# Kernel tuning notes

Hardware: AMD Instinct MI355X
Metric: run time of the kernel (lower is better)

Reference implementation:

```python
import jax, jax.numpy as jnp
import numpy as np

B, C, T = 128, 9, 2048
R = T // 4            # reduced_timesteps after two MaxPool1d(2)
N = B * R             # total graph nodes
E_SINGLE = 8192       # edges per sample graph (avg degree 16 over R nodes)
HID = 128
OUT = 12


def setup_inputs():
    key = jax.random.key(0)
    ks = jax.random.split(key, 14)
    x = jax.random.normal(ks[0], (B, C, T), jnp.float32)
    # per-sample graph, replicated with offset i*R per batch element (as in forward)
    single = jax.random.randint(ks[1], (2, E_SINGLE), 0, R)
    offsets = (jnp.arange(B) * R)[None, :, None]
    edge_index = (single[:, None, :] + offsets).reshape(2, -1)  # [2, B*E_SINGLE]

    def lin(k, fan_in, shape):
        return jax.random.normal(k, shape, jnp.float32) / np.sqrt(fan_in)

    return {
        "x": x,
        "edge_index": edge_index,
        "conv1_w": lin(ks[2], C * 5, (16, C, 5)),
        "conv1_b": jnp.zeros((16,), jnp.float32),
        "conv2_w": lin(ks[3], 16 * 5, (32, 16, 5)),
        "conv2_b": jnp.zeros((32,), jnp.float32),
        "gcn1_w": lin(ks[4], 32, (32, HID)),
        "gcn1_b": jnp.zeros((HID,), jnp.float32),
        "gcn2_w": lin(ks[5], HID, (HID, HID)),
        "gcn2_b": jnp.zeros((HID,), jnp.float32),
        "fc_w": lin(ks[6], HID, (HID, OUT)),
        "fc_b": jnp.zeros((OUT,), jnp.float32),
    }


def _gcn_conv(h, edge_index, w, b, n):
    # PyG GCNConv: linear -> add self-loops -> sym-normalized sum aggregation -> + bias
    h = h @ w
    loops = jnp.arange(n)
    row = jnp.concatenate([edge_index[0], loops])  # source
    col = jnp.concatenate([edge_index[1], loops])  # target (aggregation)
    deg = jax.ops.segment_sum(jnp.ones(col.shape, h.dtype), col, num_segments=n)
    dis = jnp.where(deg > 0, jax.lax.rsqrt(jnp.maximum(deg, 1e-12)), 0.0)
    norm = dis[row] * dis[col]                      # [E+N]
    out = jax.ops.segment_sum(norm[:, None] * h[row], col, num_segments=n)
    return out + b


def _temporal_conv(x, w1, b1, w2, b2):
    dn = ("NCH", "OIH", "NCH")
    h = jax.lax.conv_general_dilated(x, w1, (1,), [(2, 2)], dimension_numbers=dn)
    h = jax.nn.relu(h + b1[None, :, None])
    h = jax.lax.reduce_window(h, -jnp.inf, jax.lax.max, (1, 1, 2), (1, 1, 2), "VALID")
    h = jax.lax.conv_general_dilated(h, w2, (1,), [(2, 2)], dimension_numbers=dn)
    h = jax.nn.relu(h + b2[None, :, None])
    h = jax.lax.reduce_window(h, -jnp.inf, jax.lax.max, (1, 1, 2), (1, 1, 2), "VALID")
    return h  # [B, 32, R]


def reference(x, edge_index, conv1_w, conv1_b, conv2_w, conv2_b,
              gcn1_w, gcn1_b, gcn2_w, gcn2_b, fc_w, fc_b):
    h = _temporal_conv(x, conv1_w, conv1_b, conv2_w, conv2_b)   # [B, 32, R]
    nodes = h.transpose(0, 2, 1).reshape(B * R, 32)             # [N, 32]
    g = jax.nn.relu(_gcn_conv(nodes, edge_index, gcn1_w, gcn1_b, N))
    g = jax.nn.relu(_gcn_conv(g, edge_index, gcn2_w, gcn2_b, N))
    g = g.reshape(B, R, HID).mean(axis=1)                       # [B, HID]
    return g @ fc_w + fc_b                                      # [B, OUT]
```

## Files before the change

### kernel.cpp

```cpp
#include <hip/hip_runtime.h>
#include <hip/hip_bf16.h>

#define BB   128
#define CIN  9
#define TT   2048
#define RR   512
#define NN   (BB*RR)
#define HID  128
#define NOUT 12

typedef __attribute__((ext_vector_type(8))) short short8;
typedef __attribute__((ext_vector_type(4))) float f32x4;

static __device__ inline unsigned short f2bf(float f) {
    unsigned int u = __float_as_uint(f);
    unsigned int r = (u + 0x7fffu + ((u >> 16) & 1u)) >> 16;
    return (unsigned short)r;
}
static __device__ inline float bf2f(unsigned short u) {
    return __uint_as_float(((unsigned int)u) << 16);
}

__global__ __launch_bounds__(512) void k_convs(const float* __restrict__ x,
        const float* __restrict__ w1, const float* __restrict__ b1,
        const float* __restrict__ w2, const float* __restrict__ b2,
        unsigned short* __restrict__ nodesT,
        const int* __restrict__ ei, int E, int es,
        unsigned short* __restrict__ Ab16,
        const float* __restrict__ g2w, unsigned short* __restrict__ w2t,
        float* __restrict__ meanbuf, int* __restrict__ done) {
    __shared__ __align__(16) union {
        struct { float sx[CIN][268]; float s1[16][132]; } c;
        struct { int cnt[512]; float arow[8][512]; } a;
    } u;
    int tid = threadIdx.x;
    int bid = blockIdx.x;

    if (bid == 0) {
        float4 z = make_float4(0.f, 0.f, 0.f, 0.f);
        for (int i = tid; i < 128 * 128 / 4; i += 512) ((float4*)meanbuf)[i] = z;
        if (tid < 128) done[tid] = 0;
        for (int idx = tid; idx < 128 * 128; idx += 512) {
            int c2 = idx >> 7, f = idx & 127;
            w2t[f * 128 + c2] = f2bf(g2w[idx]);
        }
        return;
    }

    if (bid <= 64) {
        int base = (bid - 1) * 8;
        u.a.cnt[tid] = 0;
        float4 z = make_float4(0.f, 0.f, 0.f, 0.f);
        float4* az = (float4*)u.a.arow;
        az[tid] = z; az[tid + 512] = z;
        __syncthreads();
        for (int i = tid; i < es; i += 512) atomicAdd(&u.a.cnt[ei[E + i]], 1);
        __syncthreads();
        for (int i = tid; i < es; i += 512) {
            int c = ei[E + i];
            if (c >= base && c < base + 8) {
                int r = ei[i];
                float nd = rsqrtf((float)u.a.cnt[r] + 1.0f);
                float dn = rsqrtf((float)u.a.cnt[c] + 1.0f);
                atomicAdd(&u.a.arow[c - base][r], nd * dn);
            }
        }
        if (tid < 8) {
            int r = base + tid;
            float d = rsqrtf((float)u.a.cnt[r] + 1.0f);
            atomicAdd(&u.a.arow[tid][r], d * d);
        }
        __syncthreads();
        {
            int row = tid >> 6, c0 = (tid & 63) * 8;
            const float* p = &u.a.arow[row][c0];
            ushort4 o0, o1;
            o0.x = f2bf(p[0]); o0.y = f2bf(p[1]); o0.z = f2bf(p[2]); o0.w = f2bf(p[3]);
            o1.x = f2bf(p[4]); o1.y = f2bf(p[5]); o1.z = f2bf(p[6]); o1.w = f2bf(p[7]);
            *(ushort4*)&Ab16[(size_t)(base + row) * 512 + c0]     = o0;
            *(ushort4*)&Ab16[(size_t)(base + row) * 512 + c0 + 4] = o1;
        }
        return;
    }

    int cb = bid - 65;
    int b  = cb >> 3;
    int r0 = (cb & 7) * 64;
    int wv   = __builtin_amdgcn_readfirstlane(tid >> 6);
    int lane = tid & 63;

    for (int idx = tid; idx < CIN * 268; idx += 512) {
        int c = idx / 268, j = idx - c * 268;
        int g = 4 * r0 - 6 + j;
        float v = 0.f;
        if (g >= 0 && g < TT) v = x[(b * CIN + c) * TT + g];
        u.c.sx[c][j] = v;
    }
    __syncthreads();

    {
        int c1a = wv * 2, c1b = wv * 2 + 1;
        float biasA = b1[c1a], biasB = b1[c1b];
        for (int pp = lane; pp < 132; pp += 64) {
            int p = 2 * r0 - 2 + pp;
            float valA = 0.f, valB = 0.f;
            if (p >= 0 && p < 1024) {
                float a0A = biasA, a1A = biasA, a0B = biasB, a1B = biasB;
#pragma unroll
                for (int c = 0; c < CIN; ++c) {
                    const float2* px = (const float2*)&u.c.sx[c][2 * pp];
                    float2 q0 = px[0], q1 = px[1], q2 = px[2];
                    {
                        const float* wp = &w1[(c1a * CIN + c) * 5];
                        float k0 = wp[0], k1 = wp[1], k2 = wp[2], k3 = wp[3], k4 = wp[4];
                        a0A += q0.x*k0 + q0.y*k1 + q1.x*k2 + q1.y*k3 + q2.x*k4;
                        a1A += q0.y*k0 + q1.x*k1 + q1.y*k2 + q2.x*k3 + q2.y*k4;
                    }
                    {
                        const float* wp = &w1[(c1b * CIN + c) * 5];
                        float k0 = wp[0], k1 = wp[1], k2 = wp[2], k3 = wp[3], k4 = wp[4];
                        a0B += q0.x*k0 + q0.y*k1 + q1.x*k2 + q1.y*k3 + q2.x*k4;
                        a1B += q0.y*k0 + q1.x*k1 + q1.y*k2 + q2.x*k3 + q2.y*k4;
                    }
                }
                valA = fmaxf(fmaxf(a0A, a1A), 0.f);
                valB = fmaxf(fmaxf(a0B, a1B), 0.f);
            }
            u.c.s1[c1a][pp] = valA;
            u.c.s1[c1b][pp] = valB;
        }
    }
    __syncthreads();

    int rl = lane;
    float acc0[4], acc1[4];
#pragma unroll
    for (int o = 0; o < 4; ++o) {
        float bv = b2[wv * 4 + o];
        acc0[o] = bv; acc1[o] = bv;
    }
#pragma unroll
    for (int c = 0; c < 16; ++c) {
        const float2* ps = (const float2*)&u.c.s1[c][2 * rl];
        float2 q0 = ps[0], q1 = ps[1], q2 = ps[2];
#pragma unroll
        for (int o = 0; o < 4; ++o) {
            const float* wp = &w2[((wv * 4 + o) * 16 + c) * 5];
            float k0 = wp[0], k1 = wp[1], k2 = wp[2], k3 = wp[3], k4 = wp[4];
            acc0[o] += q0.x*k0 + q0.y*k1 + q1.x*k2 + q1.y*k3 + q2.x*k4;
            acc1[o] += q0.y*k0 + q1.x*k1 + q1.y*k2 + q2.x*k3 + q2.y*k4;
        }
    }
    int n = r0 + rl;
    unsigned short* np = nodesT + ((size_t)b * 32 + wv * 4) * 512 + n;
    np[0]    = f2bf(fmaxf(fmaxf(acc0[0], acc1[0]), 0.f));
    np[512]  = f2bf(fmaxf(fmaxf(acc0[1], acc1[1]), 0.f));
    np[1024] = f2bf(fmaxf(fmaxf(acc0[2], acc1[2]), 0.f));
    np[1536] = f2bf(fmaxf(fmaxf(acc0[3], acc1[3]), 0.f));
}

__global__ __launch_bounds__(256) void k_agg1(const unsigned short* __restrict__ Ab,
        const unsigned short* __restrict__ nT, const float* __restrict__ w1,
        const float* __restrict__ b1, unsigned short* __restrict__ h16) {
    __shared__ unsigned short sA[128][72];
    __shared__ unsigned short sN[32][72];
    __shared__ float sAgg[128][33];
    __shared__ float sw1[32 * 128];
    int tid = threadIdx.x;
    int b  = blockIdx.x >> 2;
    int rb = blockIdx.x & 3;
    int r0 = rb * 128;
    const unsigned short* nb = nT + (size_t)b * 32 * 512;

    {
        const float4* src = (const float4*)w1;
        float4* dst = (float4*)sw1;
#pragma unroll
        for (int i = 0; i < 4; ++i) dst[tid + i * 256] = src[tid + i * 256];
    }

    int wv = tid >> 6, lane = tid & 63;
    int l15 = lane & 15, quad = lane >> 4;
    int mB = wv * 32;
    f32x4 acc[2][2];
#pragma unroll
    for (int i = 0; i < 2; ++i)
#pragma unroll
        for (int j = 0; j < 2; ++j) acc[i][j] = (f32x4){0.f, 0.f, 0.f, 0.f};

    for (int kt = 0; kt < 8; ++kt) {
        int k0 = kt * 64;
        __syncthreads();
#pragma unroll
        for (int i = 0; i < 8; ++i) {
            int idx = tid + i * 256;
            int row = idx >> 4, c4 = (idx & 15) * 4;
            *(ushort4*)&sA[row][c4] = *(const ushort4*)&Ab[(size_t)(r0 + row) * 512 + k0 + c4];
        }
#pragma unroll
        for (int i = 0; i < 2; ++i) {
            int idx = tid + i * 256;
            int f = idx >> 4, c4 = (idx & 15) * 4;
            *(ushort4*)&sN[f][c4] = *(const ushort4*)&nb[(size_t)f * 512 + k0 + c4];
        }
        __syncthreads();
#pragma unroll
        for (int ks = 0; ks < 2; ++ks) {
            int kk = ks * 32 + quad * 8;
            short8 av0 = *(const short8*)&sA[mB + l15][kk];
            short8 av1 = *(const short8*)&sA[mB + 16 + l15][kk];
            short8 bv0 = *(const short8*)&sN[l15][kk];
            short8 bv1 = *(const short8*)&sN[16 + l15][kk];
            acc[0][0] = __builtin_amdgcn_mfma_f32_16x16x32_bf16(av0, bv0, acc[0][0], 0, 0, 0);
            acc[0][1] = __builtin_amdgcn_mfma_f32_16x16x32_bf16(av0, bv1, acc[0][1], 0, 0, 0);
            acc[1][0] = __builtin_amdgcn_mfma_f32_16x16x32_bf16(av1, bv0, acc[1][0], 0, 0, 0);
            acc[1][1] = __builtin_amdgcn_mfma_f32_16x16x32_bf16(av1, bv1, acc[1][1], 0, 0, 0);
        }
    }
    __syncthreads();
#pragma unroll
    for (int mi = 0; mi < 2; ++mi)
#pragma unroll
        for (int ni = 0; ni < 2; ++ni)
#pragma unroll
            for (int r = 0; r < 4; ++r)
                sAgg[mB + mi * 16 + quad * 4 + r][ni * 16 + l15] = acc[mi][ni][r];
    __syncthreads();

    int fq = tid & 31;
    int ng = tid >> 5;
    float4 bv = *(const float4*)&b1[fq * 4];
    for (int ch = 0; ch < 4; ++ch) {
        float a[4][4];
#pragma unroll
        for (int j = 0; j < 4; ++j)
#pragma unroll
            for (int q = 0; q < 4; ++q) a[j][q] = 0.f;
#pragma unroll
        for (int c = 0; c < 32; ++c) {
            float4 wvv = *(const float4*)&sw1[c * 128 + fq * 4];
#pragma unroll
            for (int j = 0; j < 4; ++j) {
                float xc = sAgg[ch * 32 + ng * 4 + j][c];
                a[j][0] += xc * wvv.x; a[j][1] += xc * wvv.y;
                a[j][2] += xc * wvv.z; a[j][3] += xc * wvv.w;
            }
        }
#pragma unroll
        for (int j = 0; j < 4; ++j) {
            ushort4 o;
            o.x = f2bf(fmaxf(a[j][0] + bv.x, 0.f));
            o.y = f2bf(fmaxf(a[j][1] + bv.y, 0.f));
            o.z = f2bf(fmaxf(a[j][2] + bv.z, 0.f));
            o.w = f2bf(fmaxf(a[j][3] + bv.w, 0.f));
            *(ushort4*)&h16[(size_t)(b * 512 + r0 + ch * 32 + ng * 4 + j) * 128 + fq * 4] = o;
        }
    }
}

__global__ __launch_bounds__(512) void k_fused2(
        const unsigned short* __restrict__ h1,
        const unsigned short* __restrict__ w2t,
        const unsigned short* __restrict__ Ab,
        const float* __restrict__ b2,
        float* __restrict__ meanbuf, int* __restrict__ done,
        const float* __restrict__ fw, const float* __restrict__ fb,
        float* __restrict__ out) {
    __shared__ __align__(16) unsigned short smem[81920];
    char* tL = (char*)smem;
    char* sS = (char*)smem + 131072;

    int tid  = threadIdx.x;
    int smp  = blockIdx.x >> 1;
    int r0   = (blockIdx.x & 1) * 256;
    int wv   = __builtin_amdgcn_readfirstlane(tid >> 6);
    int lane = tid & 63;
    int l15  = lane & 15, quad = lane >> 4;
    const unsigned short* hb = h1 + (size_t)smp * 512 * 128;

    short8 w2r[4];
#pragma unroll
    for (int ks = 0; ks < 4; ++ks)
        w2r[ks] = *(const short8*)&w2t[(wv * 16 + l15) * 128 + ks * 32 + quad * 8];

    uint4 stg[4];
#pragma unroll
    for (int i = 0; i < 4; ++i) {
        int idx = tid + i * 512;
        stg[i] = *(const uint4*)&hb[(size_t)(idx >> 4) * 128 + (idx & 15) * 8];
    }
    for (int ch = 0; ch < 4; ++ch) {
#pragma unroll
        for (int i = 0; i < 4; ++i) {
            int idx = tid + i * 512;
            int row = idx >> 4, c16 = idx & 15;
            *(uint4*)(sS + row * 256 + ((c16 ^ (row & 7)) << 4)) = stg[i];
        }
        __syncthreads();
        if (ch < 3) {
#pragma unroll
            for (int i = 0; i < 4; ++i) {
                int idx = tid + i * 512;
                stg[i] = *(const uint4*)&hb[(size_t)((ch + 1) * 128 + (idx >> 4)) * 128 + (idx & 15) * 8];
            }
        }
        f32x4 acc1[8];
#pragma unroll
        for (int nf = 0; nf < 8; ++nf) acc1[nf] = (f32x4){0.f, 0.f, 0.f, 0.f};
#pragma unroll
        for (int ks = 0; ks < 4; ++ks) {
#pragma unroll
            for (int nf = 0; nf < 8; ++nf) {
                int row = nf * 16 + l15;
                short8 hf = *(const short8*)(sS + row * 256 + (((ks * 4 + quad) ^ (row & 7)) << 4));
                acc1[nf] = __builtin_amdgcn_mfma_f32_16x16x32_bf16(w2r[ks], hf, acc1[nf], 0, 0, 0);
            }
        }
#pragma unroll
        for (int nf = 0; nf < 8; ++nf) {
#pragma unroll
            for (int r = 0; r < 4; ++r) {
                int f = wv * 16 + quad * 4 + r;
                int node = ch * 128 + nf * 16 + l15;
                *(unsigned short*)(tL + ((f * 1024 + node * 2) ^ ((f & 7) << 4))) = f2bf(acc1[nf][r]);
            }
        }
        __syncthreads();
    }

    int m_off = (wv >> 1) * 64;
    int f_off = (wv & 1) * 64;
    f32x4 acc[4][4];
#pragma unroll
    for (int i = 0; i < 4; ++i)
#pragma unroll
        for (int j = 0; j < 4; ++j) acc[i][j] = (f32x4){0.f, 0.f, 0.f, 0.f};

#pragma unroll
    for (int i = 0; i < 4; ++i) {
        int idx = tid + i * 512;
        stg[i] = *(const uint4*)&Ab[(size_t)(r0 + (idx >> 3)) * 512 + (idx & 7) * 8];
    }
    for (int kt = 0; kt < 8; ++kt) {
#pragma unroll
        for (int i = 0; i < 4; ++i) {
            int idx = tid + i * 512;
            int row = idx >> 3, c16 = idx & 7;
            *(uint4*)(sS + row * 128 + ((c16 ^ (row & 7)) << 4)) = stg[i];
        }
        __syncthreads();
        if (kt < 7) {
#pragma unroll
            for (int i = 0; i < 4; ++i) {
                int idx = tid + i * 512;
                stg[i] = *(const uint4*)&Ab[(size_t)(r0 + (idx >> 3)) * 512 + (kt + 1) * 64 + (idx & 7) * 8];
            }
        }
#pragma unroll
        for (int ks = 0; ks < 2; ++ks) {
            short8 af[4], bfr[4];
#pragma unroll
            for (int mi = 0; mi < 4; ++mi) {
                int row = m_off + mi * 16 + l15;
                af[mi] = *(const short8*)(sS + row * 128 + (((ks * 4 + quad) ^ (row & 7)) << 4));
            }
#pragma unroll
            for (int ni = 0; ni < 4; ++ni) {
                int f = f_off + ni * 16 + l15;
                int k = kt * 64 + ks * 32 + quad * 8;
                bfr[ni] = *(const short8*)(tL + ((f * 1024 + k * 2) ^ ((f & 7) << 4)));
            }
#pragma unroll
            for (int mi = 0; mi < 4; ++mi)
#pragma unroll
                for (int ni = 0; ni < 4; ++ni)
                    acc[mi][ni] = __builtin_amdgcn_mfma_f32_16x16x32_bf16(af[mi], bfr[ni], acc[mi][ni], 0, 0, 0);
        }
        __syncthreads();
    }

    float colsum[4];
#pragma unroll
    for (int ni = 0; ni < 4; ++ni) {
        int f = f_off + ni * 16 + l15;
        float bc = b2[f];
        float s = 0.f;
#pragma unroll
        for (int mi = 0; mi < 4; ++mi)
#pragma unroll
            for (int r = 0; r < 4; ++r)
                s += fmaxf(acc[mi][ni][r] + bc, 0.f);
        s += __shfl_xor(s, 16);
        s += __shfl_xor(s, 32);
        colsum[ni] = s;
    }
    float* sred = (float*)sS;
    float* smv  = sred + 512;
    int*  slastp = (int*)(smv + 128);
    if (lane < 16) {
#pragma unroll
        for (int ni = 0; ni < 4; ++ni) sred[wv * 64 + ni * 16 + lane] = colsum[ni];
    }
    __syncthreads();
    if (tid < 128) {
        int half = tid >> 6, fl = tid & 63;
        float s = sred[(half) * 64 + fl] + sred[(half + 2) * 64 + fl]
                + sred[(half + 4) * 64 + fl] + sred[(half + 6) * 64 + fl];
        atomicAdd(&meanbuf[smp * 128 + tid], s * (1.0f / RR));
    }
    __syncthreads();
    if (tid == 0) {
        __threadfence();
        *slastp = (atomicAdd(&done[smp], 1) == 1) ? 1 : 0;
    }
    __syncthreads();
    if (*slastp) {
        __threadfence();
        if (tid < HID)
            smv[tid] = __hip_atomic_load(&meanbuf[smp * 128 + tid],
                                         __ATOMIC_RELAXED, __HIP_MEMORY_SCOPE_AGENT);
        __syncthreads();
        if (tid < NOUT) {
            float s = fb[tid];
#pragma unroll
            for (int c = 0; c < HID; ++c) s += smv[c] * fw[c * NOUT + tid];
            out[smp * NOUT + tid] = s;
        }
    }
}

extern "C" void kernel_launch(void* const* d_in, const int* in_sizes, int n_in,
                              void* d_out, int out_size, void* d_ws, size_t ws_size,
                              hipStream_t stream) {
    const float* x   = (const float*)d_in[0];
    const int*   ei  = (const int*)d_in[1];
    const float* c1w = (const float*)d_in[2];
    const float* c1b = (const float*)d_in[3];
    const float* c2w = (const float*)d_in[4];
    const float* c2b = (const float*)d_in[5];
    const float* g1w = (const float*)d_in[6];
    const float* g1b = (const float*)d_in[7];
    const float* g2w = (const float*)d_in[8];
    const float* g2b = (const float*)d_in[9];
    const float* fw  = (const float*)d_in[10];
    const float* fb  = (const float*)d_in[11];
    float* out = (float*)d_out;
    int E  = in_sizes[1] / 2;
    int es = E / BB;

    char* ws = (char*)d_ws;
    unsigned short* nodesT = (unsigned short*)(ws);
    unsigned short* h1     = (unsigned short*)(ws + (4u << 20));
    unsigned short* Ab16   = (unsigned short*)(ws + (37u << 20));
    float* meanbuf         = (float*)(ws + (37u << 20) + (512u << 10));
    int*   done            = (int*)  (ws + (37u << 20) + (576u << 10));
    unsigned short* w2t    = (unsigned short*)(ws + (37u << 20) + (772u << 10));

    k_convs<<<1089, 512, 0, stream>>>(x, c1w, c1b, c2w, c2b, nodesT,
                                      ei, E, es, Ab16, g2w, w2t, meanbuf, done);

    k_agg1<<<512, 256, 0, stream>>>(Ab16, nodesT, g1w, g1b, h1);

    k_fused2<<<BB * 2, 512, 0, stream>>>(h1, w2t, Ab16, g2b,
                                         meanbuf, done, fw, fb, out);
}
```

Measured before the change: 200.5 us.

## Split second GCN layer by feature chunks across 512 smaller blocks

The fused second GCN kernel now splits each sample's work by 32-feature output chunks instead of node halves. That gives 512 blocks of 256 threads in place of 256 blocks of 512, and each block uses much less shared memory. Each block computes only its 32 features of h·W2 for all 512 nodes, reading h straight from global memory without staging it in LDS. It then multiplies the full adjacency (both row halves) against that transposed slice. This is meant to raise occupancy and spread work over more CUs. The cost is that every block reloads the whole per-sample adjacency and h tile, so global traffic goes up roughly fourfold. The completion counter is changed to wait for 4 blocks per sample.

```diff
diff --git a/kernel.cpp b/kernel.cpp
--- a/kernel.cpp
+++ b/kernel.cpp
@@ -258,7 +258,7 @@
     }
 }
 
-__global__ __launch_bounds__(512) void k_fused2(
+__global__ __launch_bounds__(256) void k_fused2(
         const unsigned short* __restrict__ h1,
         const unsigned short* __restrict__ w2t,
         const unsigned short* __restrict__ Ab,
@@ -266,155 +266,140 @@
         float* __restrict__ meanbuf, int* __restrict__ done,
         const float* __restrict__ fw, const float* __restrict__ fb,
         float* __restrict__ out) {
-    __shared__ __align__(16) unsigned short smem[81920];
-    char* tL = (char*)smem;
-    char* sS = (char*)smem + 131072;
+    __shared__ __align__(16) unsigned short tT[32][520];
+    __shared__ __align__(16) unsigned short sA[256][72];
+    __shared__ float sred[4][32];
+    __shared__ float smv[HID];
+    __shared__ int slast;
 
     int tid  = threadIdx.x;
-    int smp  = blockIdx.x >> 1;
-    int r0   = (blockIdx.x & 1) * 256;
+    int smp  = blockIdx.x & 127;
+    int fc   = blockIdx.x >> 7;
+    int f0   = fc * 32;
     int wv   = __builtin_amdgcn_readfirstlane(tid >> 6);
     int lane = tid & 63;
     int l15  = lane & 15, quad = lane >> 4;
     const unsigned short* hb = h1 + (size_t)smp * 512 * 128;
 
-    short8 w2r[4];
-#pragma unroll
-    for (int ks = 0; ks < 4; ++ks)
-        w2r[ks] = *(const short8*)&w2t[(wv * 16 + l15) * 128 + ks * 32 + quad * 8];
-
-    uint4 stg[4];
-#pragma unroll
-    for (int i = 0; i < 4; ++i) {
-        int idx = tid + i * 512;
-        stg[i] = *(const uint4*)&hb[(size_t)(idx >> 4) * 128 + (idx & 15) * 8];
-    }
-    for (int ch = 0; ch < 4; ++ch) {
-#pragma unroll
-        for (int i = 0; i < 4; ++i) {
-            int idx = tid + i * 512;
-            int row = idx >> 4, c16 = idx & 15;
-            *(uint4*)(sS + row * 256 + ((c16 ^ (row & 7)) << 4)) = stg[i];
-        }
-        __syncthreads();
-        if (ch < 3) {
-#pragma unroll
-            for (int i = 0; i < 4; ++i) {
-                int idx = tid + i * 512;
-                stg[i] = *(const uint4*)&hb[(size_t)((ch + 1) * 128 + (idx >> 4)) * 128 + (idx & 15) * 8];
-            }
-        }
-        f32x4 acc1[8];
-#pragma unroll
-        for (int nf = 0; nf < 8; ++nf) acc1[nf] = (f32x4){0.f, 0.f, 0.f, 0.f};
+    uint4 stg[8];
+#pragma unroll
+    for (int i = 0; i < 8; ++i) {
+        int idx = tid + i * 256;
+        int row = idx >> 3, c8 = idx & 7;
+        stg[i] = *(const uint4*)&Ab[(size_t)row * 512 + c8 * 8];
+    }
+
+    short8 w2r[2][4];
+#pragma unroll
+    for (int ft = 0; ft < 2; ++ft)
+#pragma unroll
+        for (int ks = 0; ks < 4; ++ks)
+            w2r[ft][ks] = *(const short8*)&w2t[(size_t)(f0 + ft * 16 + l15) * 128 + ks * 32 + quad * 8];
+
+    f32x4 acc1[2][8];
+#pragma unroll
+    for (int ft = 0; ft < 2; ++ft)
+#pragma unroll
+        for (int nt = 0; nt < 8; ++nt) acc1[ft][nt] = (f32x4){0.f, 0.f, 0.f, 0.f};
+#pragma unroll
+    for (int nt = 0; nt < 8; ++nt) {
+        int n0 = (wv * 8 + nt) * 16;
 #pragma unroll
         for (int ks = 0; ks < 4; ++ks) {
-#pragma unroll
-            for (int nf = 0; nf < 8; ++nf) {
-                int row = nf * 16 + l15;
-                short8 hf = *(const short8*)(sS + row * 256 + (((ks * 4 + quad) ^ (row & 7)) << 4));
-                acc1[nf] = __builtin_amdgcn_mfma_f32_16x16x32_bf16(w2r[ks], hf, acc1[nf], 0, 0, 0);
-            }
-        }
-#pragma unroll
-        for (int nf = 0; nf < 8; ++nf) {
-#pragma unroll
-            for (int r = 0; r < 4; ++r) {
-                int f = wv * 16 + quad * 4 + r;
-                int node = ch * 128 + nf * 16 + l15;
-                *(unsigned short*)(tL + ((f * 1024 + node * 2) ^ ((f & 7) << 4))) = f2bf(acc1[nf][r]);
-            }
-        }
-        __syncthreads();
-    }
-
-    int m_off = (wv >> 1) * 64;
-    int f_off = (wv & 1) * 64;
-    f32x4 acc[4][4];
-#pragma unroll
-    for (int i = 0; i < 4; ++i)
-#pragma unroll
-        for (int j = 0; j < 4; ++j) acc[i][j] = (f32x4){0.f, 0.f, 0.f, 0.f};
-
-#pragma unroll
-    for (int i = 0; i < 4; ++i) {
-        int idx = tid + i * 512;
-        stg[i] = *(const uint4*)&Ab[(size_t)(r0 + (idx >> 3)) * 512 + (idx & 7) * 8];
-    }
-    for (int kt = 0; kt < 8; ++kt) {
-#pragma unroll
-        for (int i = 0; i < 4; ++i) {
-            int idx = tid + i * 512;
-            int row = idx >> 3, c16 = idx & 7;
-            *(uint4*)(sS + row * 128 + ((c16 ^ (row & 7)) << 4)) = stg[i];
-        }
-        __syncthreads();
-        if (kt < 7) {
-#pragma unroll
-            for (int i = 0; i < 4; ++i) {
-                int idx = tid + i * 512;
-                stg[i] = *(const uint4*)&Ab[(size_t)(r0 + (idx >> 3)) * 512 + (kt + 1) * 64 + (idx & 7) * 8];
-            }
-        }
-#pragma unroll
-        for (int ks = 0; ks < 2; ++ks) {
-            short8 af[4], bfr[4];
-#pragma unroll
-            for (int mi = 0; mi < 4; ++mi) {
-                int row = m_off + mi * 16 + l15;
-                af[mi] = *(const short8*)(sS + row * 128 + (((ks * 4 + quad) ^ (row & 7)) << 4));
-            }
-#pragma unroll
-            for (int ni = 0; ni < 4; ++ni) {
-                int f = f_off + ni * 16 + l15;
-                int k = kt * 64 + ks * 32 + quad * 8;
-                bfr[ni] = *(const short8*)(tL + ((f * 1024 + k * 2) ^ ((f & 7) << 4)));
-            }
-#pragma unroll
-            for (int mi = 0; mi < 4; ++mi)
-#pragma unroll
-                for (int ni = 0; ni < 4; ++ni)
-                    acc[mi][ni] = __builtin_amdgcn_mfma_f32_16x16x32_bf16(af[mi], bfr[ni], acc[mi][ni], 0, 0, 0);
-        }
-        __syncthreads();
-    }
-
-    float colsum[4];
-#pragma unroll
-    for (int ni = 0; ni < 4; ++ni) {
-        int f = f_off + ni * 16 + l15;
-        float bc = b2[f];
-        float s = 0.f;
+            short8 hf = *(const short8*)&hb[(size_t)(n0 + l15) * 128 + ks * 32 + quad * 8];
+            acc1[0][nt] = __builtin_amdgcn_mfma_f32_16x16x32_bf16(w2r[0][ks], hf, acc1[0][nt], 0, 0, 0);
+            acc1[1][nt] = __builtin_amdgcn_mfma_f32_16x16x32_bf16(w2r[1][ks], hf, acc1[1][nt], 0, 0, 0);
+        }
+    }
+#pragma unroll
+    for (int ft = 0; ft < 2; ++ft)
+#pragma unroll
+        for (int nt = 0; nt < 8; ++nt) {
+            int node = (wv * 8 + nt) * 16 + l15;
+#pragma unroll
+            for (int r = 0; r < 4; ++r)
+                tT[ft * 16 + quad * 4 + r][node] = f2bf(acc1[ft][nt][r]);
+        }
+    __syncthreads();
+
+    float bias[2];
+#pragma unroll
+    for (int ft = 0; ft < 2; ++ft) bias[ft] = b2[f0 + ft * 16 + l15];
+    float colsum[2] = {0.f, 0.f};
+
+    for (int mc = 0; mc < 2; ++mc) {
+        f32x4 acc[4][2];
 #pragma unroll
         for (int mi = 0; mi < 4; ++mi)
 #pragma unroll
-            for (int r = 0; r < 4; ++r)
-                s += fmaxf(acc[mi][ni][r] + bc, 0.f);
+            for (int ft = 0; ft < 2; ++ft) acc[mi][ft] = (f32x4){0.f, 0.f, 0.f, 0.f};
+
+        for (int kt = 0; kt < 8; ++kt) {
+#pragma unroll
+            for (int i = 0; i < 8; ++i) {
+                int idx = tid + i * 256;
+                int row = idx >> 3, c8 = idx & 7;
+                *(uint4*)&sA[row][c8 * 8] = stg[i];
+            }
+            __syncthreads();
+            if (!(mc == 1 && kt == 7)) {
+                int nmc = (kt == 7) ? 1 : mc;
+                int nkt = (kt == 7) ? 0 : kt + 1;
+#pragma unroll
+                for (int i = 0; i < 8; ++i) {
+                    int idx = tid + i * 256;
+                    int row = idx >> 3, c8 = idx & 7;
+                    stg[i] = *(const uint4*)&Ab[(size_t)(nmc * 256 + row) * 512 + nkt * 64 + c8 * 8];
+                }
+            }
+#pragma unroll
+            for (int ks = 0; ks < 2; ++ks) {
+                int kk = ks * 32 + quad * 8;
+                short8 af[4], bf[2];
+#pragma unroll
+                for (int mi = 0; mi < 4; ++mi)
+                    af[mi] = *(const short8*)&sA[wv * 64 + mi * 16 + l15][kk];
+#pragma unroll
+                for (int ft = 0; ft < 2; ++ft)
+                    bf[ft] = *(const short8*)&tT[ft * 16 + l15][kt * 64 + kk];
+#pragma unroll
+                for (int mi = 0; mi < 4; ++mi)
+#pragma unroll
+                    for (int ft = 0; ft < 2; ++ft)
+                        acc[mi][ft] = __builtin_amdgcn_mfma_f32_16x16x32_bf16(af[mi], bf[ft], acc[mi][ft], 0, 0, 0);
+            }
+            __syncthreads();
+        }
+#pragma unroll
+        for (int mi = 0; mi < 4; ++mi)
+#pragma unroll
+            for (int ft = 0; ft < 2; ++ft) {
+                float s = 0.f;
+#pragma unroll
+                for (int r = 0; r < 4; ++r)
+                    s += fmaxf(acc[mi][ft][r] + bias[ft], 0.f);
+                colsum[ft] += s;
+            }
+    }
+
+#pragma unroll
+    for (int ft = 0; ft < 2; ++ft) {
+        float s = colsum[ft];
         s += __shfl_xor(s, 16);
         s += __shfl_xor(s, 32);
-        colsum[ni] = s;
-    }
-    float* sred = (float*)sS;
-    float* smv  = sred + 512;
-    int*  slastp = (int*)(smv + 128);
-    if (lane < 16) {
-#pragma unroll
-        for (int ni = 0; ni < 4; ++ni) sred[wv * 64 + ni * 16 + lane] = colsum[ni];
-    }
-    __syncthreads();
-    if (tid < 128) {
-        int half = tid >> 6, fl = tid & 63;
-        float s = sred[(half) * 64 + fl] + sred[(half + 2) * 64 + fl]
-                + sred[(half + 4) * 64 + fl] + sred[(half + 6) * 64 + fl];
-        atomicAdd(&meanbuf[smp * 128 + tid], s * (1.0f / RR));
-    }
+        if (quad == 0) sred[wv][ft * 16 + l15] = s;
+    }
+    __syncthreads();
+    if (tid < 32)
+        atomicAdd(&meanbuf[smp * 128 + f0 + tid],
+                  (sred[0][tid] + sred[1][tid] + sred[2][tid] + sred[3][tid]) * (1.0f / RR));
     __syncthreads();
     if (tid == 0) {
         __threadfence();
-        *slastp = (atomicAdd(&done[smp], 1) == 1) ? 1 : 0;
-    }
-    __syncthreads();
-    if (*slastp) {
+        slast = (atomicAdd(&done[smp], 1) == 3) ? 1 : 0;
+    }
+    __syncthreads();
+    if (slast) {
         __threadfence();
         if (tid < HID)
             smv[tid] = __hip_atomic_load(&meanbuf[smp * 128 + tid],
@@ -461,6 +446,6 @@
 
     k_agg1<<<512, 256, 0, stream>>>(Ab16, nodesT, g1w, g1b, h1);
 
-    k_fused2<<<BB * 2, 512, 0, stream>>>(h1, w2t, Ab16, g2b,
-                                         meanbuf, done, fw, fb, out);
-}
+    k_fused2<<<512, 256, 0, stream>>>(h1, w2t, Ab16, g2b,
+                                      meanbuf, done, fw, fb, out);
+}
```

After: 234.8 us. 1.17x slower.
